# Kernel optimization log

Measured on AMD Instinct MI355X. Metric: run time of the kernel, lower is better.

Reference implementation:

```python
import jax, jax.numpy as jnp
import numpy as np

B, C, H, W = 4, 256, 64, 64
HALF = C // 2
BN_EPS = 1e-5


def setup_inputs() -> dict:
    key = jax.random.key(0)
    ks = jax.random.split(key, 6)
    scale = 1.0 / np.sqrt(C)
    return {
        "x": jax.random.normal(ks[0], (B, C, H, W), dtype=jnp.float32),
        "w1": jax.random.normal(ks[1], (HALF, C), dtype=jnp.float32) * scale,
        "w2": jax.random.normal(ks[2], (HALF, C), dtype=jnp.float32) * scale,
        "w3": jax.random.normal(ks[3], (HALF, C), dtype=jnp.float32) * scale,
        "w4": jax.random.normal(ks[4], (C, HALF), dtype=jnp.float32) * (1.0 / np.sqrt(HALF)),
        "gamma": jnp.ones((C,), dtype=jnp.float32),
        "beta": jnp.zeros((C,), dtype=jnp.float32),
        "running_mean": jnp.zeros((C,), dtype=jnp.float32),
        "running_var": jnp.ones((C,), dtype=jnp.float32),
    }


def _conv1x1(x, w):
    # x: [b,c,h,w], w: [out,in] -> [b,out,h,w]
    return jnp.einsum('bchw,oc->bohw', x, w)


def reference(x, w1, w2, w3, w4, gamma, beta, running_mean, running_var):
    b, Cin, h, w = x.shape
    c = Cin // 2
    hw = h * w
    n1 = _conv1x1(x, w1)  # [b,c,h,w]
    n2 = _conv1x1(x, w2)
    n3 = _conv1x1(x, w3)
    # Faithful to torch .view (raw reshape, NOT a transpose)
    q = n1.reshape(b, hw, c)   # [b,hw,c]
    k = n2.reshape(b, c, hw)   # [b,c,hw]
    attn = jnp.einsum('bic,bcj->bij', q, k)        # [b,hw,hw]
    attn = jax.nn.softmax(attn, axis=-1)
    v = n3.reshape(b, hw, c)
    res = jnp.einsum('bij,bjc->bic', attn, v)      # [b,hw,c]
    res = res.reshape(b, c, h, w)
    out = _conv1x1(res, w4)                        # [b,C,h,w]
    # BatchNorm2d in eval mode with running stats
    inv = jax.lax.rsqrt(running_var + BN_EPS)
    out = (out - running_mean[None, :, None, None]) * (gamma * inv)[None, :, None, None] + beta[None, :, None, None]
    return out + x
```

## Files before the change

kernel.cpp:

```cpp
#include <hip/hip_runtime.h>
#include <cstdint>

#define BN 4
#define CIN 256
#define HALFC 128
#define HW 4096
#define SPLIT 4
#define JT 64
#define JITERS (HW / SPLIT / JT)

typedef float  floatx4 __attribute__((ext_vector_type(4)));
typedef short  shortx8 __attribute__((ext_vector_type(8)));

#if __has_builtin(__builtin_amdgcn_exp2f)
#define EXP2F(x) __builtin_amdgcn_exp2f(x)
#else
#define EXP2F(x) exp2f(x)
#endif
#define L2E 1.44269504088896f

__device__ __forceinline__ unsigned short f2bf(float f) {
  unsigned u = __float_as_uint(f);
  u += 0x7FFFu + ((u >> 16) & 1u);
  return (unsigned short)(u >> 16);
}

__device__ __forceinline__ void async16(const void* g, void* l) {
  __builtin_amdgcn_global_load_lds((const __attribute__((address_space(1))) void*)g,
                                   (__attribute__((address_space(3))) void*)l, 16, 0, 0);
}

__global__ __launch_bounds__(256) void k_split(const float* __restrict__ x,
    const float* __restrict__ w1, const float* __restrict__ w2,
    const float* __restrict__ w3, unsigned short* __restrict__ Xth,
    unsigned short* __restrict__ Wh) {
  __shared__ float smf[64 * 65];
  int bid = blockIdx.x;
  int t = threadIdx.x;
  if (bid < 1024) {
    int b = bid >> 8, rem = bid & 255;
    int cit = rem >> 6, pxt = rem & 63;
    const float* src = x + (size_t)b * 1048576 + (size_t)(cit * 64) * HW + pxt * 64;
#pragma unroll
    for (int k = 0; k < 16; k++) {
      int idx = k * 256 + t;
      int r = idx >> 6, c = idx & 63;
      smf[r * 65 + c] = src[(size_t)r * HW + c];
    }
    __syncthreads();
    int prow = t >> 2, seg = t & 3;
    union { unsigned short us[16]; uint4 v[2]; } oh;
#pragma unroll
    for (int u = 0; u < 16; u++)
      oh.us[u] = f2bf(smf[(seg * 16 + u) * 65 + prow]);
    size_t dst = (size_t)b * 1048576 + (size_t)(pxt * 64 + prow) * 256 + cit * 64 + seg * 16;
    *(uint4*)(Xth + dst) = oh.v[0];
    *(uint4*)(Xth + dst + 8) = oh.v[1];
  } else {
    int bw = bid - 1024;
    int f0 = bw * 8192 + t * 32;
    const float* wsrc;
    int fo;
    if (f0 < 32768)      { wsrc = w1; fo = f0; }
    else if (f0 < 65536) { wsrc = w2; fo = f0 - 32768; }
    else                 { wsrc = w3; fo = f0 - 65536; }
    union { unsigned short us[32]; uint4 v[4]; } oh;
#pragma unroll
    for (int u = 0; u < 32; u++) oh.us[u] = f2bf(wsrc[fo + u]);
#pragma unroll
    for (int k = 0; k < 4; k++) *((uint4*)(Wh + f0) + k) = oh.v[k];
  }
}

__global__ __launch_bounds__(256) void k_projM(const unsigned short* __restrict__ Xth,
    const unsigned short* __restrict__ Wh, unsigned short* __restrict__ Q,
    unsigned short* __restrict__ Kt, unsigned short* __restrict__ n3) {
  __shared__ unsigned short XhS[3 * 4096];
  __shared__ unsigned short ES[9216];
  int bid = blockIdx.x;
  int pxt = bid & 31;
  int ct = bid >> 5;
  int b = ct / 6, cot = ct % 6;
  int px0 = pxt * 128, co0 = cot * 64;
  int t = threadIdx.x;
  int w = t >> 6, lane = t & 63, l16 = lane & 15, quad = lane >> 4;

  int myco = co0 + w * 16 + l16;
  shortx8 whf[8];
#pragma unroll
  for (int s = 0; s < 8; s++)
    whf[s] = *(const shortx8*)(Wh + (size_t)myco * 256 + s * 32 + quad * 8);
  floatx4 acc[8];
  floatx4 zf = {0.f, 0.f, 0.f, 0.f};
#pragma unroll
  for (int mt = 0; mt < 8; mt++) acc[mt] = zf;
  const unsigned short* XhB = Xth + (size_t)b * 1048576;
  int k8 = lane >> 4, pxm = lane & 15;

#pragma unroll
  for (int c2 = 0; c2 < 2; c2++) {
    int px = px0 + (c2 * 4 + w) * 16 + pxm;
    async16(XhB + (size_t)px * 256 + k8 * 8, (char*)XhS + c2 * 4096 + w * 1024);
  }

#pragma unroll
  for (int s = 0; s < 8; s++) {
    if (s + 1 < 8) {
      int nb = (s + 1) % 3;
#pragma unroll
      for (int c2 = 0; c2 < 2; c2++) {
        int px = px0 + (c2 * 4 + w) * 16 + pxm;
        async16(XhB + (size_t)px * 256 + (s + 1) * 32 + k8 * 8,
                (char*)XhS + nb * 8192 + c2 * 4096 + w * 1024);
      }
      __asm__ __volatile__("s_waitcnt vmcnt(2)" ::: "memory");
    } else {
      __asm__ __volatile__("s_waitcnt vmcnt(0)" ::: "memory");
    }
    __asm__ __volatile__("s_barrier" ::: "memory");
    const char* cb = (const char*)XhS + (s % 3) * 8192;
#pragma unroll
    for (int mt = 0; mt < 8; mt++) {
      shortx8 ah = *(const shortx8*)(cb + mt * 1024 + lane * 16);
      acc[mt] = __builtin_amdgcn_mfma_f32_16x16x32_bf16(ah, whf[s], acc[mt], 0, 0, 0);
    }
  }
  __syncthreads();
  if (cot < 2 || cot >= 4) {
    int co_l = w * 16 + l16;
#pragma unroll
    for (int mt = 0; mt < 8; mt++) {
      int px = mt * 16 + quad * 4;
      unsigned lo = (unsigned)f2bf(acc[mt][0]) | ((unsigned)f2bf(acc[mt][1]) << 16);
      unsigned hi = (unsigned)f2bf(acc[mt][2]) | ((unsigned)f2bf(acc[mt][3]) << 16);
      *(uint2*)(ES + co_l * 136 + px) = make_uint2(lo, hi);
    }
    __syncthreads();
    int cr = t >> 2, seg = t & 3;
    unsigned short* dstb = (cot < 2)
        ? Q  + (size_t)b * 524288 + (size_t)(co0 + cr) * HW
        : n3 + (size_t)b * 524288 + (size_t)(co0 - 256 + cr) * HW;
#pragma unroll
    for (int k2 = 0; k2 < 4; k2++) {
      uint4 v = *(const uint4*)(ES + cr * 136 + seg * 32 + k2 * 8);
      *(uint4*)(dstb + px0 + seg * 32 + k2 * 8) = v;
    }
  } else {
#pragma unroll
    for (int mt = 0; mt < 8; mt++)
#pragma unroll
      for (int rr = 0; rr < 4; rr++) {
        int px = mt * 16 + quad * 4 + rr;
        ES[px * 72 + w * 16 + l16] = f2bf(acc[mt][rr]);
      }
    __syncthreads();
    int ch0 = co0 - 128;
#pragma unroll
    for (int it = 0; it < 4; it++) {
      int cid = it * 256 + t;
      int px = cid >> 3, c8 = cid & 7;
      uint4 v = *(const uint4*)(ES + px * 72 + c8 * 8);
      *(uint4*)(Kt + (size_t)b * 524288 + (size_t)(px0 + px) * 128 + ch0 + c8 * 8) = v;
    }
  }
}

__global__ __launch_bounds__(256) void k_layoutVF(const unsigned short* __restrict__ n3,
    unsigned short* __restrict__ VtF) {
  __shared__ unsigned short sm[8192];
  int bid = blockIdx.x;
  int b = bid >> 6, jt = bid & 63;
  int t = threadIdx.x;
  const unsigned short* src = n3 + (size_t)b * 524288 + (size_t)(jt * 2) * 4096;
#pragma unroll
  for (int k = 0; k < 4; k++) {
    int idx = k * 256 + t;
    ((uint4*)sm)[idx] = ((const uint4*)src)[idx];
  }
  __syncthreads();
  unsigned short* dst = VtF + (size_t)b * 524288 + (size_t)jt * 8192;
#pragma unroll
  for (int k = 0; k < 4; k++) {
    int s = k * 256 + t;
    int nt = s >> 7, kt = (s >> 6) & 1, quad = (s >> 4) & 3, l16 = s & 15;
    union { unsigned short us[8]; uint4 v; } o;
#pragma unroll
    for (int e = 0; e < 8; e++)
      o.us[e] = sm[kt * 4096 + (quad * 8 + e) * 128 + nt * 16 + l16];
    *(uint4*)(dst + s * 8) = o.v;
  }
}

__global__ __launch_bounds__(256, 2) void k_flash(const unsigned short* __restrict__ Q,
    const unsigned short* __restrict__ Kt, const unsigned short* __restrict__ VtF,
    float* __restrict__ Opart, float* __restrict__ ml) {
  __shared__ unsigned short KtS[2 * 8192];
  __shared__ unsigned short VS[2 * 8192];
  __shared__ unsigned short PS[4 * 2048];
  int bid0 = blockIdx.x;
  int bid = (bid0 & 7) * 64 + (bid0 >> 3);
  int itile = bid & 31, sp = (bid >> 5) & 3, b = bid >> 7;
  int t = threadIdx.x;
  int w = t >> 6, lane = t & 63, l16 = lane & 15, quad = lane >> 4;
  int i0 = itile * 128;

  shortx8 qf[2][4];
#pragma unroll
  for (int ig = 0; ig < 2; ig++) {
    const unsigned short* qp = Q + ((size_t)b * HW + i0 + w * 32 + ig * 16 + l16) * 128 + quad * 8;
#pragma unroll
    for (int ks = 0; ks < 4; ks++) qf[ig][ks] = *(const shortx8*)(qp + ks * 32);
  }
  __asm__ __volatile__("s_waitcnt vmcnt(0)" ::: "memory");

  floatx4 O[2][8];
  floatx4 zf = {0.f, 0.f, 0.f, 0.f};
#pragma unroll
  for (int ig = 0; ig < 2; ig++)
#pragma unroll
    for (int nt = 0; nt < 8; nt++) O[ig][nt] = zf;
  float m_i[2] = {-1e30f, -1e30f}, l_i[2] = {0.f, 0.f};

  int ccK = w * 4 + quad;
  const unsigned short* kbase = Kt + (size_t)b * HW * 128
                              + (size_t)(sp * 1024 + l16) * 128 + ccK * 8;
  const unsigned short* vbase = VtF + (size_t)b * 524288 + (size_t)(sp * 16) * 8192
                              + w * 512 + lane * 8;
  char* Pw = (char*)PS + w * 4096;

#pragma unroll
  for (int c4 = 0; c4 < 4; c4++) {
    async16(kbase + c4 * 2048, (char*)KtS + c4 * 4096 + w * 1024);
    async16(vbase + c4 * 2048, (char*)VS + c4 * 4096 + w * 1024);
  }

  for (int it = 0; it < JITERS; it++) {
    int cur = it & 1, nxt = cur ^ 1;
    if (it + 1 < JITERS) {
      const unsigned short* kp = kbase + (size_t)(it + 1) * 8192;
#pragma unroll
      for (int c4 = 0; c4 < 4; c4++)
        async16(kp + c4 * 2048, (char*)KtS + nxt * 16384 + c4 * 4096 + w * 1024);
      __asm__ __volatile__("s_waitcnt vmcnt(4)" ::: "memory");
    } else {
      __asm__ __volatile__("s_waitcnt vmcnt(0)" ::: "memory");
    }
    __asm__ __volatile__("s_barrier" ::: "memory");
    __asm__ __volatile__("s_waitcnt lgkmcnt(0)" ::: "memory");

    const char* kc = (const char*)KtS + cur * 16384;

    floatx4 S[2][4];
#pragma unroll
    for (int ig = 0; ig < 2; ig++)
#pragma unroll
      for (int mt = 0; mt < 4; mt++) S[ig][mt] = zf;
    __builtin_amdgcn_s_setprio(1);
    if (it > 0) {
      const char* vp = (const char*)VS + nxt * 16384;
#pragma unroll
      for (int kt = 0; kt < 2; kt++) {
        shortx8 pf0 = *(const shortx8*)(Pw + kt * 1024 + lane * 16);
        shortx8 pf1 = *(const shortx8*)(Pw + 2048 + kt * 1024 + lane * 16);
#pragma unroll
        for (int nt = 0; nt < 8; nt++) {
          shortx8 vfr = *(const shortx8*)(vp + ((nt * 2 + kt) * 64 + lane) * 16);
          O[0][nt] = __builtin_amdgcn_mfma_f32_16x16x32_bf16(pf0, vfr, O[0][nt], 0, 0, 0);
          O[1][nt] = __builtin_amdgcn_mfma_f32_16x16x32_bf16(pf1, vfr, O[1][nt], 0, 0, 0);
        }
      }
    }
#pragma unroll
    for (int mt = 0; mt < 4; mt++) {
#pragma unroll
      for (int ks = 0; ks < 4; ks++) {
        shortx8 af = *(const shortx8*)(kc + mt * 4096 + ks * 1024 + lane * 16);
        S[0][mt] = __builtin_amdgcn_mfma_f32_16x16x32_bf16(af, qf[0][ks], S[0][mt], 0, 0, 0);
        S[1][mt] = __builtin_amdgcn_mfma_f32_16x16x32_bf16(af, qf[1][ks], S[1][mt], 0, 0, 0);
      }
    }
    __builtin_amdgcn_s_setprio(0);
    __asm__ __volatile__("s_barrier" ::: "memory");
    if (it + 1 < JITERS) {
      const unsigned short* vp2 = vbase + (size_t)(it + 1) * 8192;
#pragma unroll
      for (int c4 = 0; c4 < 4; c4++)
        async16(vp2 + c4 * 2048, (char*)VS + nxt * 16384 + c4 * 4096 + w * 1024);
    }

    float tmax[2];
#pragma unroll
    for (int ig = 0; ig < 2; ig++) {
      float a0 = fmaxf(fmaxf(S[ig][0][0], S[ig][0][1]), fmaxf(S[ig][0][2], S[ig][0][3]));
      float a1 = fmaxf(fmaxf(S[ig][1][0], S[ig][1][1]), fmaxf(S[ig][1][2], S[ig][1][3]));
      float a2 = fmaxf(fmaxf(S[ig][2][0], S[ig][2][1]), fmaxf(S[ig][2][2], S[ig][2][3]));
      float a3 = fmaxf(fmaxf(S[ig][3][0], S[ig][3][1]), fmaxf(S[ig][3][2], S[ig][3][3]));
      float tm = fmaxf(fmaxf(a0, a1), fmaxf(a2, a3));
      tm = fmaxf(tm, __shfl_xor(tm, 16));
      tm = fmaxf(tm, __shfl_xor(tm, 32));
      tmax[ig] = tm;
    }
    float alpha[2] = {1.f, 1.f};
    if (__ballot(tmax[0] > m_i[0] + 8.f || tmax[1] > m_i[1] + 8.f)) {
#pragma unroll
      for (int ig = 0; ig < 2; ig++) {
        float mn = fmaxf(m_i[ig], tmax[ig]);
        alpha[ig] = EXP2F((m_i[ig] - mn) * L2E);
        m_i[ig] = mn;
        float ar[4];
#pragma unroll
        for (int rr = 0; rr < 4; rr++) ar[rr] = __shfl(alpha[ig], quad * 4 + rr);
#pragma unroll
        for (int nt = 0; nt < 8; nt++)
#pragma unroll
          for (int rr = 0; rr < 4; rr++) O[ig][nt][rr] *= ar[rr];
      }
    }
#pragma unroll
    for (int ig = 0; ig < 2; ig++) {
      float nsc = m_i[ig] * L2E;
      float sm[4];
#pragma unroll
      for (int mt = 0; mt < 4; mt++) {
        float p0 = EXP2F(fmaf(S[ig][mt][0], L2E, -nsc));
        float p1 = EXP2F(fmaf(S[ig][mt][1], L2E, -nsc));
        float p2 = EXP2F(fmaf(S[ig][mt][2], L2E, -nsc));
        float p3 = EXP2F(fmaf(S[ig][mt][3], L2E, -nsc));
        S[ig][mt][0] = p0; S[ig][mt][1] = p1; S[ig][mt][2] = p2; S[ig][mt][3] = p3;
        sm[mt] = (p0 + p1) + (p2 + p3);
      }
      float ts = (sm[0] + sm[1]) + (sm[2] + sm[3]);
      ts += __shfl_xor(ts, 16);
      ts += __shfl_xor(ts, 32);
      l_i[ig] = l_i[ig] * alpha[ig] + ts;
#pragma unroll
      for (int mt = 0; mt < 4; mt++) {
        unsigned lo = __builtin_amdgcn_perm(__float_as_uint(S[ig][mt][1]),
                                            __float_as_uint(S[ig][mt][0]), 0x07060302u);
        unsigned hi = __builtin_amdgcn_perm(__float_as_uint(S[ig][mt][3]),
                                            __float_as_uint(S[ig][mt][2]), 0x07060302u);
        *(uint2*)(Pw + ig * 2048 + (mt * 2 + (quad >> 1)) * 256 + l16 * 16 + (quad & 1) * 8)
            = make_uint2(lo, hi);
      }
    }
  }
  __asm__ __volatile__("s_waitcnt lgkmcnt(0)" ::: "memory");
  {
    const char* vp = (const char*)VS + ((JITERS - 1) & 1) * 16384;
#pragma unroll
    for (int kt = 0; kt < 2; kt++) {
      shortx8 pf0 = *(const shortx8*)(Pw + kt * 1024 + lane * 16);
      shortx8 pf1 = *(const shortx8*)(Pw + 2048 + kt * 1024 + lane * 16);
#pragma unroll
      for (int nt = 0; nt < 8; nt++) {
        shortx8 vfr = *(const shortx8*)(vp + ((nt * 2 + kt) * 64 + lane) * 16);
        O[0][nt] = __builtin_amdgcn_mfma_f32_16x16x32_bf16(pf0, vfr, O[0][nt], 0, 0, 0);
        O[1][nt] = __builtin_amdgcn_mfma_f32_16x16x32_bf16(pf1, vfr, O[1][nt], 0, 0, 0);
      }
    }
  }
#pragma unroll
  for (int ig = 0; ig < 2; ig++) {
    float* Ob = Opart + ((size_t)(sp * 4 + b) * HW + i0 + w * 32 + ig * 16) * 128;
#pragma unroll
    for (int nt = 0; nt < 8; nt++)
#pragma unroll
      for (int rr = 0; rr < 4; rr++)
        Ob[(size_t)(quad * 4 + rr) * 128 + nt * 16 + l16] = O[ig][nt][rr];
  }
  if (quad == 0) {
    float2* mlp = (float2*)ml;
#pragma unroll
    for (int ig = 0; ig < 2; ig++)
      mlp[(size_t)(sp * 4 + b) * HW + i0 + w * 32 + ig * 16 + l16]
          = make_float2(m_i[ig], l_i[ig]);
  }
}

__global__ __launch_bounds__(256) void k_merge(const float* __restrict__ Opart,
    const float* __restrict__ ml, float* __restrict__ res) {
  size_t e = (size_t)blockIdx.x * 256 + threadIdx.x;
  int cq = (int)(e & 31);
  int i = (int)((e >> 5) & 4095);
  int b = (int)(e >> 17);
  const float2* mlp = (const float2*)ml;
  float m[SPLIT], l[SPLIT];
  float M = -1e30f;
#pragma unroll
  for (int s = 0; s < SPLIT; s++) {
    float2 st = mlp[(size_t)(s * 4 + b) * HW + i];
    m[s] = st.x; l[s] = st.y;
    M = fmaxf(M, m[s]);
  }
  float denom = 0.f;
  float wgt[SPLIT];
#pragma unroll
  for (int s = 0; s < SPLIT; s++) {
    float ws_ = EXP2F((m[s] - M) * L2E);
    wgt[s] = ws_;
    denom += l[s] * ws_;
  }
  float inv = 1.f / denom;
  floatx4 acc = {0.f, 0.f, 0.f, 0.f};
#pragma unroll
  for (int s = 0; s < SPLIT; s++) {
    floatx4 v = *(const floatx4*)(Opart + ((size_t)(s * 4 + b) * HW + i) * 128 + cq * 4);
    acc += v * (wgt[s] * inv);
  }
  *(floatx4*)(res + e * 4) = acc;
}

__global__ __launch_bounds__(256) void k_out(const float* __restrict__ res,
    const float* __restrict__ w4, const float* __restrict__ gamma,
    const float* __restrict__ beta, const float* __restrict__ rmean,
    const float* __restrict__ rvar, const float* __restrict__ x,
    float* __restrict__ out) {
  __shared__ float wt[16 * 128];
  int bid = blockIdx.x;
  int cot = bid & 15;
  int st = (bid >> 4) & 15;
  int b = bid >> 8;
  int t = threadIdx.x;
  int co0 = cot * 16;
#pragma unroll
  for (int k = 0; k < 8; k++) wt[k * 256 + t] = w4[(size_t)co0 * 128 + k * 256 + t];
  __syncthreads();
  int px = st * 256 + t;
  const float* rb = res + (size_t)b * 524288 + px;
  float acc[16];
#pragma unroll
  for (int r = 0; r < 16; r++) acc[r] = 0.f;
  for (int ci = 0; ci < 128; ci += 4) {
    float xv[4];
#pragma unroll
    for (int kk = 0; kk < 4; kk++) xv[kk] = rb[(size_t)(ci + kk) * HW];
#pragma unroll
    for (int r = 0; r < 16; r++) {
      floatx4 wv = *(const floatx4*)&wt[r * 128 + ci];
#pragma unroll
      for (int kk = 0; kk < 4; kk++) acc[r] += wv[kk] * xv[kk];
    }
  }
  const float* xb = x + ((size_t)b * 256 + co0) * HW + px;
  float* ob = out + ((size_t)b * 256 + co0) * HW + px;
#pragma unroll
  for (int r = 0; r < 16; r++) {
    int co = co0 + r;
    float g = gamma[co] * rsqrtf(rvar[co] + 1e-5f);
    float bb = beta[co] - rmean[co] * g;
    ob[(size_t)r * HW] = acc[r] * g + bb + xb[(size_t)r * HW];
  }
}

extern "C" void kernel_launch(void* const* d_in, const int* in_sizes, int n_in,
                              void* d_out, int out_size, void* d_ws, size_t ws_size,
                              hipStream_t stream) {
  const float* x     = (const float*)d_in[0];
  const float* w1    = (const float*)d_in[1];
  const float* w2    = (const float*)d_in[2];
  const float* w3    = (const float*)d_in[3];
  const float* w4    = (const float*)d_in[4];
  const float* gamma = (const float*)d_in[5];
  const float* beta  = (const float*)d_in[6];
  const float* rmean = (const float*)d_in[7];
  const float* rvar  = (const float*)d_in[8];
  float* out = (float*)d_out;
  char* ws = (char*)d_ws;

  size_t off = (size_t)SPLIT * 4 * HW * 128 * 4;
  float* Opart = (float*)ws;
  unsigned short* n3  = (unsigned short*)ws;
  unsigned short* Xth = (unsigned short*)(ws + ((size_t)8 << 20));
  unsigned short* Q   = (unsigned short*)(ws + off); off += (size_t)4 * HW * 128 * 2;
  unsigned short* Kt  = (unsigned short*)(ws + off); off += (size_t)4 * HW * 128 * 2;
  unsigned short* VtF = (unsigned short*)(ws + off); off += (size_t)4 * HW * 128 * 2;
  float* ml  = (float*)(ws + off); off += (size_t)SPLIT * 4 * HW * 2 * 4;
  float* res = (float*)(ws + off); off += (size_t)4 * HW * 128 * 4;
  unsigned short* Wh = (unsigned short*)(ws + off); off += (size_t)384 * 256 * 2;
  if (ws_size < off) return;

  k_split   <<<1036, 256, 0, stream>>>(x, w1, w2, w3, Xth, Wh);
  k_projM   <<<768,  256, 0, stream>>>(Xth, Wh, Q, Kt, n3);
  k_layoutVF<<<256,  256, 0, stream>>>(n3, VtF);
  k_flash   <<<512,  256, 0, stream>>>(Q, Kt, VtF, Opart, ml);
  k_merge   <<<2048, 256, 0, stream>>>(Opart, ml, res);
  k_out     <<<1024, 256, 0, stream>>>(res, w4, gamma, beta, rmean, rvar, x, out);
}
```

Baseline: 188.3 us.

## Fuse V layout into projection and split-merge into output conv

The projection kernel now writes the V projection straight into the fragment layout the flash kernel expects, which removes the separate n3 buffer and the layout kernel. The split-K merge is folded into the output 1x1 conv kernel. Each block computes per-row merge weights from the m/l statistics into shared memory and combines the four partial outputs on the fly while reading them. This removes two launches and the round trips through the res and n3 intermediates, in exchange for scattered 2-byte stores for V and four partial-output loads per input element in the output kernel.

```diff
diff --git a/kernel.cpp b/kernel.cpp
--- a/kernel.cpp
+++ b/kernel.cpp
@@ -74,7 +74,7 @@
 
 __global__ __launch_bounds__(256) void k_projM(const unsigned short* __restrict__ Xth,
     const unsigned short* __restrict__ Wh, unsigned short* __restrict__ Q,
-    unsigned short* __restrict__ Kt, unsigned short* __restrict__ n3) {
+    unsigned short* __restrict__ Kt, unsigned short* __restrict__ VtF) {
   __shared__ unsigned short XhS[3 * 4096];
   __shared__ unsigned short ES[9216];
   int bid = blockIdx.x;
@@ -125,8 +125,8 @@
       acc[mt] = __builtin_amdgcn_mfma_f32_16x16x32_bf16(ah, whf[s], acc[mt], 0, 0, 0);
     }
   }
-  __syncthreads();
-  if (cot < 2 || cot >= 4) {
+  if (cot < 2) {
+    __syncthreads();
     int co_l = w * 16 + l16;
 #pragma unroll
     for (int mt = 0; mt < 8; mt++) {
@@ -137,15 +137,14 @@
     }
     __syncthreads();
     int cr = t >> 2, seg = t & 3;
-    unsigned short* dstb = (cot < 2)
-        ? Q  + (size_t)b * 524288 + (size_t)(co0 + cr) * HW
-        : n3 + (size_t)b * 524288 + (size_t)(co0 - 256 + cr) * HW;
+    unsigned short* dstb = Q + (size_t)b * 524288 + (size_t)(co0 + cr) * HW;
 #pragma unroll
     for (int k2 = 0; k2 < 4; k2++) {
       uint4 v = *(const uint4*)(ES + cr * 136 + seg * 32 + k2 * 8);
       *(uint4*)(dstb + px0 + seg * 32 + k2 * 8) = v;
     }
-  } else {
+  } else if (cot < 4) {
+    __syncthreads();
 #pragma unroll
     for (int mt = 0; mt < 8; mt++)
 #pragma unroll
@@ -162,32 +161,15 @@
       uint4 v = *(const uint4*)(ES + px * 72 + c8 * 8);
       *(uint4*)(Kt + (size_t)b * 524288 + (size_t)(px0 + px) * 128 + ch0 + c8 * 8) = v;
     }
-  }
-}
-
-__global__ __launch_bounds__(256) void k_layoutVF(const unsigned short* __restrict__ n3,
-    unsigned short* __restrict__ VtF) {
-  __shared__ unsigned short sm[8192];
-  int bid = blockIdx.x;
-  int b = bid >> 6, jt = bid & 63;
-  int t = threadIdx.x;
-  const unsigned short* src = n3 + (size_t)b * 524288 + (size_t)(jt * 2) * 4096;
-#pragma unroll
-  for (int k = 0; k < 4; k++) {
-    int idx = k * 256 + t;
-    ((uint4*)sm)[idx] = ((const uint4*)src)[idx];
-  }
-  __syncthreads();
-  unsigned short* dst = VtF + (size_t)b * 524288 + (size_t)jt * 8192;
-#pragma unroll
-  for (int k = 0; k < 4; k++) {
-    int s = k * 256 + t;
-    int nt = s >> 7, kt = (s >> 6) & 1, quad = (s >> 4) & 3, l16 = s & 15;
-    union { unsigned short us[8]; uint4 v; } o;
-#pragma unroll
-    for (int e = 0; e < 8; e++)
-      o.us[e] = sm[kt * 4096 + (quad * 8 + e) * 128 + nt * 16 + l16];
-    *(uint4*)(dst + s * 8) = o.v;
+  } else {
+    int cop = (cot - 4) * 64 + w * 16 + l16;
+    unsigned short* vb2 = VtF + (size_t)b * 524288 + (size_t)(cop >> 1) * 8192
+                        + (cop & 1) * 512 + (pxt >> 3) * 128 + quad * 32 + (pxt & 7);
+#pragma unroll
+    for (int mt = 0; mt < 8; mt++)
+#pragma unroll
+      for (int rr = 0; rr < 4; rr++)
+        vb2[mt * 1024 + rr * 8] = f2bf(acc[mt][rr]);
   }
 }
 
@@ -377,45 +359,13 @@
   }
 }
 
-__global__ __launch_bounds__(256) void k_merge(const float* __restrict__ Opart,
-    const float* __restrict__ ml, float* __restrict__ res) {
-  size_t e = (size_t)blockIdx.x * 256 + threadIdx.x;
-  int cq = (int)(e & 31);
-  int i = (int)((e >> 5) & 4095);
-  int b = (int)(e >> 17);
-  const float2* mlp = (const float2*)ml;
-  float m[SPLIT], l[SPLIT];
-  float M = -1e30f;
-#pragma unroll
-  for (int s = 0; s < SPLIT; s++) {
-    float2 st = mlp[(size_t)(s * 4 + b) * HW + i];
-    m[s] = st.x; l[s] = st.y;
-    M = fmaxf(M, m[s]);
-  }
-  float denom = 0.f;
-  float wgt[SPLIT];
-#pragma unroll
-  for (int s = 0; s < SPLIT; s++) {
-    float ws_ = EXP2F((m[s] - M) * L2E);
-    wgt[s] = ws_;
-    denom += l[s] * ws_;
-  }
-  float inv = 1.f / denom;
-  floatx4 acc = {0.f, 0.f, 0.f, 0.f};
-#pragma unroll
-  for (int s = 0; s < SPLIT; s++) {
-    floatx4 v = *(const floatx4*)(Opart + ((size_t)(s * 4 + b) * HW + i) * 128 + cq * 4);
-    acc += v * (wgt[s] * inv);
-  }
-  *(floatx4*)(res + e * 4) = acc;
-}
-
-__global__ __launch_bounds__(256) void k_out(const float* __restrict__ res,
-    const float* __restrict__ w4, const float* __restrict__ gamma,
-    const float* __restrict__ beta, const float* __restrict__ rmean,
-    const float* __restrict__ rvar, const float* __restrict__ x,
-    float* __restrict__ out) {
+__global__ __launch_bounds__(256) void k_mergeout(const float* __restrict__ Opart,
+    const float* __restrict__ ml, const float* __restrict__ w4,
+    const float* __restrict__ gamma, const float* __restrict__ beta,
+    const float* __restrict__ rmean, const float* __restrict__ rvar,
+    const float* __restrict__ x, float* __restrict__ out) {
   __shared__ float wt[16 * 128];
+  __shared__ __align__(16) float tblws[256 * 4];
   int bid = blockIdx.x;
   int cot = bid & 15;
   int st = (bid >> 4) & 15;
@@ -424,16 +374,51 @@
   int co0 = cot * 16;
 #pragma unroll
   for (int k = 0; k < 8; k++) wt[k * 256 + t] = w4[(size_t)co0 * 128 + k * 256 + t];
+  {
+    int ip = (t >> 1) * 32 + st * 2 + (t & 1);
+    const float2* mlp = (const float2*)ml;
+    float m[SPLIT], l[SPLIT];
+    float M = -1e30f;
+#pragma unroll
+    for (int s = 0; s < SPLIT; s++) {
+      float2 v = mlp[(size_t)(s * 4 + b) * HW + ip];
+      m[s] = v.x; l[s] = v.y;
+      M = fmaxf(M, m[s]);
+    }
+    float denom = 0.f;
+    float wgt[SPLIT];
+#pragma unroll
+    for (int s = 0; s < SPLIT; s++) {
+      float ws_ = EXP2F((m[s] - M) * L2E);
+      wgt[s] = ws_;
+      denom += l[s] * ws_;
+    }
+    float inv = 1.f / denom;
+    floatx4 wsv = {wgt[0] * inv, wgt[1] * inv, wgt[2] * inv, wgt[3] * inv};
+    *(floatx4*)&tblws[t * 4] = wsv;
+  }
   __syncthreads();
   int px = st * 256 + t;
-  const float* rb = res + (size_t)b * 524288 + px;
+  int half = t >> 7;
+  const float* Op0 = Opart + (size_t)(0 * 4 + b) * 524288 + px;
+  const float* Op1 = Opart + (size_t)(1 * 4 + b) * 524288 + px;
+  const float* Op2 = Opart + (size_t)(2 * 4 + b) * 524288 + px;
+  const float* Op3 = Opart + (size_t)(3 * 4 + b) * 524288 + px;
   float acc[16];
 #pragma unroll
   for (int r = 0; r < 16; r++) acc[r] = 0.f;
   for (int ci = 0; ci < 128; ci += 4) {
     float xv[4];
 #pragma unroll
-    for (int kk = 0; kk < 4; kk++) xv[kk] = rb[(size_t)(ci + kk) * HW];
+    for (int kk = 0; kk < 4; kk++) {
+      floatx4 wsv = *(const floatx4*)&tblws[((ci + kk) * 2 + half) * 4];
+      size_t o = (size_t)(ci + kk) * HW;
+      float v = Op0[o] * wsv[0];
+      v = fmaf(Op1[o], wsv[1], v);
+      v = fmaf(Op2[o], wsv[2], v);
+      v = fmaf(Op3[o], wsv[3], v);
+      xv[kk] = v;
+    }
 #pragma unroll
     for (int r = 0; r < 16; r++) {
       floatx4 wv = *(const floatx4*)&wt[r * 128 + ci];
@@ -469,20 +454,16 @@
 
   size_t off = (size_t)SPLIT * 4 * HW * 128 * 4;
   float* Opart = (float*)ws;
-  unsigned short* n3  = (unsigned short*)ws;
   unsigned short* Xth = (unsigned short*)(ws + ((size_t)8 << 20));
   unsigned short* Q   = (unsigned short*)(ws + off); off += (size_t)4 * HW * 128 * 2;
   unsigned short* Kt  = (unsigned short*)(ws + off); off += (size_t)4 * HW * 128 * 2;
   unsigned short* VtF = (unsigned short*)(ws + off); off += (size_t)4 * HW * 128 * 2;
   float* ml  = (float*)(ws + off); off += (size_t)SPLIT * 4 * HW * 2 * 4;
-  float* res = (float*)(ws + off); off += (size_t)4 * HW * 128 * 4;
   unsigned short* Wh = (unsigned short*)(ws + off); off += (size_t)384 * 256 * 2;
   if (ws_size < off) return;
 
   k_split   <<<1036, 256, 0, stream>>>(x, w1, w2, w3, Xth, Wh);
-  k_projM   <<<768,  256, 0, stream>>>(Xth, Wh, Q, Kt, n3);
-  k_layoutVF<<<256,  256, 0, stream>>>(n3, VtF);
+  k_projM   <<<768,  256, 0, stream>>>(Xth, Wh, Q, Kt, VtF);
   k_flash   <<<512,  256, 0, stream>>>(Q, Kt, VtF, Opart, ml);
-  k_merge   <<<2048, 256, 0, stream>>>(Opart, ml, res);
-  k_out     <<<1024, 256, 0, stream>>>(res, w4, gamma, beta, rmean, rvar, x, out);
-}
+  k_mergeout<<<1024, 256, 0, stream>>>(Opart, ml, w4, gamma, beta, rmean, rvar, x, out);
+}
```

New measurement: 200.2 us. 6.3% more time.

## Fuse split-softmax merge into output projection and BN residual kernel

Applied to the files above, without the earlier changes.

Replaces the separate merge kernel and the 1x1 output-conv kernel with a single kernel. Each block computes per-row merge weights for its 32 pixels into shared memory, combines the four partial outputs directly into an LDS tile, then runs the w4 projection with folded BatchNorm and the residual add. This removes the fp32 res intermediate round trip through global memory and one launch. In exchange it reloads w4 chunks once per block, uses less per-thread accumulation, and has more __syncthreads.

```diff
diff --git a/kernel.cpp b/kernel.cpp
--- a/kernel.cpp
+++ b/kernel.cpp
@@ -377,78 +377,83 @@
   }
 }
 
-__global__ __launch_bounds__(256) void k_merge(const float* __restrict__ Opart,
-    const float* __restrict__ ml, float* __restrict__ res) {
-  size_t e = (size_t)blockIdx.x * 256 + threadIdx.x;
-  int cq = (int)(e & 31);
-  int i = (int)((e >> 5) & 4095);
-  int b = (int)(e >> 17);
-  const float2* mlp = (const float2*)ml;
-  float m[SPLIT], l[SPLIT];
-  float M = -1e30f;
-#pragma unroll
-  for (int s = 0; s < SPLIT; s++) {
-    float2 st = mlp[(size_t)(s * 4 + b) * HW + i];
-    m[s] = st.x; l[s] = st.y;
-    M = fmaxf(M, m[s]);
-  }
-  float denom = 0.f;
-  float wgt[SPLIT];
-#pragma unroll
-  for (int s = 0; s < SPLIT; s++) {
-    float ws_ = EXP2F((m[s] - M) * L2E);
-    wgt[s] = ws_;
-    denom += l[s] * ws_;
-  }
-  float inv = 1.f / denom;
-  floatx4 acc = {0.f, 0.f, 0.f, 0.f};
-#pragma unroll
-  for (int s = 0; s < SPLIT; s++) {
-    floatx4 v = *(const floatx4*)(Opart + ((size_t)(s * 4 + b) * HW + i) * 128 + cq * 4);
-    acc += v * (wgt[s] * inv);
-  }
-  *(floatx4*)(res + e * 4) = acc;
-}
-
-__global__ __launch_bounds__(256) void k_out(const float* __restrict__ res,
-    const float* __restrict__ w4, const float* __restrict__ gamma,
-    const float* __restrict__ beta, const float* __restrict__ rmean,
-    const float* __restrict__ rvar, const float* __restrict__ x,
-    float* __restrict__ out) {
-  __shared__ float wt[16 * 128];
+__global__ __launch_bounds__(256) void k_mergeout(const float* __restrict__ Opart,
+    const float* __restrict__ ml, const float* __restrict__ w4,
+    const float* __restrict__ gamma, const float* __restrict__ beta,
+    const float* __restrict__ rmean, const float* __restrict__ rvar,
+    const float* __restrict__ x, float* __restrict__ out) {
+  __shared__ float xm[128 * 32];
+  __shared__ float wtc[32 * 128];
+  __shared__ __align__(16) float tbl[128 * 4];
   int bid = blockIdx.x;
-  int cot = bid & 15;
-  int st = (bid >> 4) & 15;
-  int b = bid >> 8;
+  int st = bid & 127, b = bid >> 7;
   int t = threadIdx.x;
-  int co0 = cot * 16;
-#pragma unroll
-  for (int k = 0; k < 8; k++) wt[k * 256 + t] = w4[(size_t)co0 * 128 + k * 256 + t];
+  int px0 = st * 32;
+  if (t < 128) {
+    int ip = t * 32 + (st >> 2);
+    const float2* mlp = (const float2*)ml;
+    float m[SPLIT], l[SPLIT];
+    float M = -1e30f;
+#pragma unroll
+    for (int s = 0; s < SPLIT; s++) {
+      float2 v = mlp[(size_t)(s * 4 + b) * HW + ip];
+      m[s] = v.x; l[s] = v.y;
+      M = fmaxf(M, m[s]);
+    }
+    float denom = 0.f;
+    float wgt[SPLIT];
+#pragma unroll
+    for (int s = 0; s < SPLIT; s++) {
+      float ws_ = EXP2F((m[s] - M) * L2E);
+      wgt[s] = ws_;
+      denom += l[s] * ws_;
+    }
+    float inv = 1.f / denom;
+    floatx4 wsv = {wgt[0] * inv, wgt[1] * inv, wgt[2] * inv, wgt[3] * inv};
+    *(floatx4*)&tbl[t * 4] = wsv;
+  }
   __syncthreads();
-  int px = st * 256 + t;
-  const float* rb = res + (size_t)b * 524288 + px;
-  float acc[16];
-#pragma unroll
-  for (int r = 0; r < 16; r++) acc[r] = 0.f;
-  for (int ci = 0; ci < 128; ci += 4) {
-    float xv[4];
-#pragma unroll
-    for (int kk = 0; kk < 4; kk++) xv[kk] = rb[(size_t)(ci + kk) * HW];
-#pragma unroll
-    for (int r = 0; r < 16; r++) {
-      floatx4 wv = *(const floatx4*)&wt[r * 128 + ci];
-#pragma unroll
-      for (int kk = 0; kk < 4; kk++) acc[r] += wv[kk] * xv[kk];
-    }
-  }
-  const float* xb = x + ((size_t)b * 256 + co0) * HW + px;
-  float* ob = out + ((size_t)b * 256 + co0) * HW + px;
-#pragma unroll
-  for (int r = 0; r < 16; r++) {
-    int co = co0 + r;
-    float g = gamma[co] * rsqrtf(rvar[co] + 1e-5f);
-    float bb = beta[co] - rmean[co] * g;
-    ob[(size_t)r * HW] = acc[r] * g + bb + xb[(size_t)r * HW];
+  const float* Op0 = Opart + (size_t)(0 * 4 + b) * 524288 + px0;
+  const float* Op1 = Opart + (size_t)(1 * 4 + b) * 524288 + px0;
+  const float* Op2 = Opart + (size_t)(2 * 4 + b) * 524288 + px0;
+  const float* Op3 = Opart + (size_t)(3 * 4 + b) * 524288 + px0;
+#pragma unroll
+  for (int k = 0; k < 16; k++) {
+    int idx = k * 256 + t;
+    int ci = idx >> 5, pxl = idx & 31;
+    floatx4 wsv = *(const floatx4*)&tbl[ci * 4];
+    size_t o = (size_t)ci * HW + pxl;
+    float v = Op0[o] * wsv[0];
+    v = fmaf(Op1[o], wsv[1], v);
+    v = fmaf(Op2[o], wsv[2], v);
+    v = fmaf(Op3[o], wsv[3], v);
+    xm[idx] = v;
+  }
+  int pxl = t & 31, cog = t >> 5;
+  int px = px0 + pxl;
+  for (int c8 = 0; c8 < 8; c8++) {
+    __syncthreads();
+#pragma unroll
+    for (int k = 0; k < 16; k++) {
+      int idx = k * 256 + t;
+      wtc[idx] = w4[c8 * 4096 + idx];
+    }
+    __syncthreads();
+    float acc[4] = {0.f, 0.f, 0.f, 0.f};
+    for (int ci = 0; ci < 128; ci++) {
+      float xv = xm[ci * 32 + pxl];
+#pragma unroll
+      for (int r = 0; r < 4; r++)
+        acc[r] = fmaf(wtc[(cog * 4 + r) * 128 + ci], xv, acc[r]);
+    }
+#pragma unroll
+    for (int r = 0; r < 4; r++) {
+      int co = c8 * 32 + cog * 4 + r;
+      float g = gamma[co] * rsqrtf(rvar[co] + 1e-5f);
+      float bb = beta[co] - rmean[co] * g;
+      size_t oo = ((size_t)(b * 256 + co)) * HW + px;
+      out[oo] = acc[r] * g + bb + x[oo];
+    }
   }
 }
 
@@ -475,7 +480,6 @@
   unsigned short* Kt  = (unsigned short*)(ws + off); off += (size_t)4 * HW * 128 * 2;
   unsigned short* VtF = (unsigned short*)(ws + off); off += (size_t)4 * HW * 128 * 2;
   float* ml  = (float*)(ws + off); off += (size_t)SPLIT * 4 * HW * 2 * 4;
-  float* res = (float*)(ws + off); off += (size_t)4 * HW * 128 * 4;
   unsigned short* Wh = (unsigned short*)(ws + off); off += (size_t)384 * 256 * 2;
   if (ws_size < off) return;
 
@@ -483,6 +487,5 @@
   k_projM   <<<768,  256, 0, stream>>>(Xth, Wh, Q, Kt, n3);
   k_layoutVF<<<256,  256, 0, stream>>>(n3, VtF);
   k_flash   <<<512,  256, 0, stream>>>(Q, Kt, VtF, Opart, ml);
-  k_merge   <<<2048, 256, 0, stream>>>(Opart, ml, res);
-  k_out     <<<1024, 256, 0, stream>>>(res, w4, gamma, beta, rmean, rvar, x, out);
-}
+  k_mergeout<<<512,  256, 0, stream>>>(Opart, ml, w4, gamma, beta, rmean, rvar, x, out);
+}
```

New measurement: 188.4 us. Within noise of the previous version (+0.1%).
